# Optimization experiments

Measured on AMD Instinct MI355X. Metric: run time of the kernel, lower is better.

The kernel has to match this reference:

```python
import jax, jax.numpy as jnp
import numpy as np

ALPHA = 0.2  # LeakyReLU negative slope


def setup_inputs() -> dict:
    key = jax.random.key(0)
    k1, k2, k3, k4 = jax.random.split(key, 4)
    N, F_in, F_out = 8192, 512, 64
    x = jax.random.normal(k1, (N, F_in), dtype=jnp.float32)
    adj = jax.random.uniform(k2, (N, N), dtype=jnp.float32)
    W = jax.random.normal(k3, (F_in, F_out), dtype=jnp.float32) * 0.05
    a = jax.random.normal(k4, (2 * F_out, 1), dtype=jnp.float32) * 0.05
    return {"x": x, "adj": adj, "W": W, "a": a}


def reference(x, adj, W, a):
    F_out = W.shape[1]
    h = x @ W                                   # [N, F_out]
    # Additive attention decomposed: score[i,j] = h[i]·a1 + h[j]·a2
    # (equivalent to concat([h_i, h_j]) @ a, without the N×N×2F blowup)
    a1 = a[:F_out, 0]                           # [F_out]
    a2 = a[F_out:, 0]                           # [F_out]
    e = jax.nn.leaky_relu(h @ a1[:, None] + (h @ a2)[None, :], ALPHA)  # [N, N]
    attention = jax.nn.softmax(e * adj, axis=1)  # elementwise mult, as in source
    # dropout skipped (eval / training=False -> identity)
    h_prime = attention @ h                      # [N, F_out]
    return jax.nn.elu(h_prime)                   # concat=True branch
```

## Files before the change

kernel.cpp:

```cpp
#include <hip/hip_runtime.h>

#define ALPHA 0.2f

typedef __attribute__((ext_vector_type(8))) short short8v;
typedef __attribute__((ext_vector_type(4))) float f32x4;

__device__ __forceinline__ unsigned cvt_pk_bf16(float a, float b) {
  unsigned d;
  asm("v_cvt_pk_bf16_f32 %0, %1, %2" : "=v"(d) : "v"(a), "v"(b));
  return d;
}

__global__ __launch_bounds__(256) void k1_proj(
    const float* __restrict__ x, const float* __restrict__ W,
    const float* __restrict__ avec,
    short* __restrict__ hT, float* __restrict__ s1, float* __restrict__ s2) {
  __shared__ float xl[32 * 132];
  __shared__ float Wl[128 * 64];
  const int t   = threadIdx.x;
  const int rb  = blockIdx.x;
  const int row = t >> 3;
  const int fg  = t & 7;
  float acc[8];
#pragma unroll
  for (int e = 0; e < 8; e++) acc[e] = 0.f;

  for (int kc = 0; kc < 4; kc++) {
#pragma unroll
    for (int u = 0; u < 4; u++) {
      int lin = t + u * 256;
      int r = lin >> 5, c4 = lin & 31;
      float4 v = *(const float4*)(x + (size_t)(rb * 32 + r) * 512 + kc * 128 + c4 * 4);
      *(float4*)(xl + r * 132 + c4 * 4) = v;
    }
#pragma unroll
    for (int u = 0; u < 8; u++) {
      int lin = t + u * 256;
      int r = lin >> 4, c4 = lin & 15;
      float4 v = *(const float4*)(W + (size_t)(kc * 128 + r) * 64 + c4 * 4);
      *(float4*)(Wl + r * 64 + c4 * 4) = v;
    }
    __syncthreads();
#pragma unroll 8
    for (int k = 0; k < 128; k++) {
      float xv = xl[row * 132 + k];
      float4 w0 = *(const float4*)(Wl + k * 64 + fg * 8);
      float4 w1 = *(const float4*)(Wl + k * 64 + fg * 8 + 4);
      acc[0] = fmaf(xv, w0.x, acc[0]); acc[1] = fmaf(xv, w0.y, acc[1]);
      acc[2] = fmaf(xv, w0.z, acc[2]); acc[3] = fmaf(xv, w0.w, acc[3]);
      acc[4] = fmaf(xv, w1.x, acc[4]); acc[5] = fmaf(xv, w1.y, acc[5]);
      acc[6] = fmaf(xv, w1.z, acc[6]); acc[7] = fmaf(xv, w1.w, acc[7]);
    }
    __syncthreads();
  }

  float p1 = 0.f, p2 = 0.f;
#pragma unroll
  for (int e = 0; e < 8; e++) {
    p1 = fmaf(acc[e], avec[fg * 8 + e], p1);
    p2 = fmaf(acc[e], avec[64 + fg * 8 + e], p2);
  }
  p1 += __shfl_xor(p1, 1, 64); p1 += __shfl_xor(p1, 2, 64); p1 += __shfl_xor(p1, 4, 64);
  p2 += __shfl_xor(p2, 1, 64); p2 += __shfl_xor(p2, 2, 64); p2 += __shfl_xor(p2, 4, 64);
  const int gi = rb * 32 + row;
  if (fg == 0) { s1[gi] = p1; s2[gi] = p2; }
#pragma unroll
  for (int e = 0; e < 8; e++) {
    union { float f; unsigned u; } v; v.f = acc[e];
    unsigned rr = v.u + 0x7fffu + ((v.u >> 16) & 1u);
    hT[(size_t)(fg * 8 + e) * 8192 + gi] = (short)(rr >> 16);
  }
}

__global__ __launch_bounds__(256, 2) void k2_attn(
    const float* __restrict__ adj, const short* __restrict__ hT,
    const float* __restrict__ s1, const float* __restrict__ s2,
    float* __restrict__ num, float* __restrict__ den) {
  __shared__ short hP[32768];
  __shared__ short Pl[8192];
  const int t    = threadIdx.x;
  const int wvi  = t >> 6;
  const int l    = t & 63;
  const int lq   = l >> 4;
  const int lr   = l & 15;
  const int rb   = blockIdx.x & 127;
  const int ks   = blockIdx.x >> 7;
  const int r0   = rb << 6;
  const int j0   = ks << 9;

  float  s1own = s1[r0 + wvi * 16 + lr];
  float4 s2A4  = *(const float4*)(s2 + j0 + l * 4);
  float4 s2B4  = *(const float4*)(s2 + j0 + 256 + l * 4);

  short8v sv[16];
#pragma unroll
  for (int r = 0; r < 16; r++) {
    const int d    = r * 4096 + t * 16;
    const int frow = d >> 10;
    const int lcb  = (d & 1023) ^ ((frow & 7) << 4);
    sv[r] = *(const short8v*)(hT + (size_t)frow * 8192 + j0 + (lcb >> 1));
  }

  const float* ar = adj + (size_t)(r0 + wvi * 16) * 8192 + j0 + l * 4;
  float4 A0,A1,A2,A3,A4,A5,A6,A7,A8,A9,A10,A11,A12,A13,A14,A15;
  float4 B0,B1,B2,B3,B4,B5,B6,B7,B8,B9,B10,B11,B12,B13,B14,B15;
  A0  = *(const float4*)(ar);              B0  = *(const float4*)(ar + 256);
  A1  = *(const float4*)(ar + 1 * 8192);   B1  = *(const float4*)(ar + 1 * 8192 + 256);
  A2  = *(const float4*)(ar + 2 * 8192);   B2  = *(const float4*)(ar + 2 * 8192 + 256);
  A3  = *(const float4*)(ar + 3 * 8192);   B3  = *(const float4*)(ar + 3 * 8192 + 256);
  A4  = *(const float4*)(ar + 4 * 8192);   B4  = *(const float4*)(ar + 4 * 8192 + 256);
  A5  = *(const float4*)(ar + 5 * 8192);   B5  = *(const float4*)(ar + 5 * 8192 + 256);
  A6  = *(const float4*)(ar + 6 * 8192);   B6  = *(const float4*)(ar + 6 * 8192 + 256);
  A7  = *(const float4*)(ar + 7 * 8192);   B7  = *(const float4*)(ar + 7 * 8192 + 256);
  A8  = *(const float4*)(ar + 8 * 8192);   B8  = *(const float4*)(ar + 8 * 8192 + 256);
  A9  = *(const float4*)(ar + 9 * 8192);   B9  = *(const float4*)(ar + 9 * 8192 + 256);
  A10 = *(const float4*)(ar + 10 * 8192);  B10 = *(const float4*)(ar + 10 * 8192 + 256);
  A11 = *(const float4*)(ar + 11 * 8192);  B11 = *(const float4*)(ar + 11 * 8192 + 256);
  A12 = *(const float4*)(ar + 12 * 8192);  B12 = *(const float4*)(ar + 12 * 8192 + 256);
  A13 = *(const float4*)(ar + 13 * 8192);  B13 = *(const float4*)(ar + 13 * 8192 + 256);
  A14 = *(const float4*)(ar + 14 * 8192);  B14 = *(const float4*)(ar + 14 * 8192 + 256);
  A15 = *(const float4*)(ar + 15 * 8192);  B15 = *(const float4*)(ar + 15 * 8192 + 256);

#pragma unroll
  for (int r = 0; r < 16; r++)
    *(short8v*)((char*)hP + r * 4096 + t * 16) = sv[r];
  __syncthreads();

  float s1r[16];
#pragma unroll
  for (int i = 0; i < 16; i++) s1r[i] = __shfl(s1own, i, 64);

  float denom_p[16];
#pragma unroll
  for (int i = 0; i < 16; i++) denom_p[i] = 0.f;
  f32x4 acc[4];
#pragma unroll
  for (int fb = 0; fb < 4; fb++) acc[fb] = (f32x4){0.f, 0.f, 0.f, 0.f};

  char* Pw = (char*)Pl + wvi * 4096;
  unsigned pk0[16], pk1[16];

#define EXPROW4(I, AV, S2V) do {                                              \
    float z0 = s1r[I] + S2V.x; z0 = fmaxf(z0, ALPHA * z0) * AV.x;             \
    float z1 = s1r[I] + S2V.y; z1 = fmaxf(z1, ALPHA * z1) * AV.y;             \
    float z2 = s1r[I] + S2V.z; z2 = fmaxf(z2, ALPHA * z2) * AV.z;             \
    float z3 = s1r[I] + S2V.w; z3 = fmaxf(z3, ALPHA * z3) * AV.w;             \
    float w0 = __expf(z0), w1 = __expf(z1), w2 = __expf(z2), w3 = __expf(z3); \
    denom_p[I] += (w0 + w1) + (w2 + w3);                                      \
    pk0[I] = cvt_pk_bf16(w0, w1); pk1[I] = cvt_pk_bf16(w2, w3);               \
  } while (0)

#define PWRITE(HALF) do {                                                     \
    if ((l >> 5) == (HALF)) {                                                 \
      const int cb = (l & 31) * 8;                                            \
      _Pragma("unroll")                                                       \
      for (int i2 = 0; i2 < 16; i2++) {                                       \
        uint2 pv; pv.x = pk0[i2]; pv.y = pk1[i2];                             \
        *(uint2*)(Pw + (((i2 << 8) + cb) ^ ((i2 & 7) << 4))) = pv;            \
      }                                                                       \
    }                                                                         \
  } while (0)

#define MFMACHUNK(CL) do {                                                    \
    __builtin_amdgcn_s_setprio(1);                                            \
    _Pragma("unroll")                                                         \
    for (int kk = 0; kk < 4; kk++) {                                          \
      const int ab = ((lr << 8) + (kk << 6) + (lq << 4)) ^ ((lr & 7) << 4);   \
      const short8v au = *(const short8v*)(Pw + ab);                          \
      _Pragma("unroll")                                                       \
      for (int fb = 0; fb < 4; fb++) {                                        \
        const int fr = fb * 16 + lr;                                          \
        const int bb = ((fr << 10) + ((CL) << 8) + (kk << 6) + (lq << 4))     \
                       ^ ((fr & 7) << 4);                                     \
        const short8v bu = *(const short8v*)((char*)hP + bb);                 \
        acc[fb] = __builtin_amdgcn_mfma_f32_16x16x32_bf16(au, bu,             \
                                                          acc[fb], 0, 0, 0); \
      }                                                                       \
    }                                                                         \
    __builtin_amdgcn_s_setprio(0);                                            \
  } while (0)

  EXPROW4(0, A0, s2A4);   EXPROW4(1, A1, s2A4);   EXPROW4(2, A2, s2A4);
  EXPROW4(3, A3, s2A4);   EXPROW4(4, A4, s2A4);   EXPROW4(5, A5, s2A4);
  EXPROW4(6, A6, s2A4);   EXPROW4(7, A7, s2A4);   EXPROW4(8, A8, s2A4);
  EXPROW4(9, A9, s2A4);   EXPROW4(10, A10, s2A4); EXPROW4(11, A11, s2A4);
  EXPROW4(12, A12, s2A4); EXPROW4(13, A13, s2A4); EXPROW4(14, A14, s2A4);
  EXPROW4(15, A15, s2A4);
  PWRITE(0); MFMACHUNK(0);
  PWRITE(1); MFMACHUNK(1);

  EXPROW4(0, B0, s2B4);   EXPROW4(1, B1, s2B4);   EXPROW4(2, B2, s2B4);
  EXPROW4(3, B3, s2B4);   EXPROW4(4, B4, s2B4);   EXPROW4(5, B5, s2B4);
  EXPROW4(6, B6, s2B4);   EXPROW4(7, B7, s2B4);   EXPROW4(8, B8, s2B4);
  EXPROW4(9, B9, s2B4);   EXPROW4(10, B10, s2B4); EXPROW4(11, B11, s2B4);
  EXPROW4(12, B12, s2B4); EXPROW4(13, B13, s2B4); EXPROW4(14, B14, s2B4);
  EXPROW4(15, B15, s2B4);
  PWRITE(0); MFMACHUNK(2);
  PWRITE(1); MFMACHUNK(3);

#undef EXPROW4
#undef PWRITE
#undef MFMACHUNK

#pragma unroll
  for (int i = 0; i < 16; i++) {
    float d = denom_p[i];
    d += __shfl_xor(d, 1, 64); d += __shfl_xor(d, 2, 64);
    d += __shfl_xor(d, 4, 64); d += __shfl_xor(d, 8, 64);
    d += __shfl_xor(d, 16, 64); d += __shfl_xor(d, 32, 64);
    if (l == 0) den[(size_t)ks * 8192 + r0 + wvi * 16 + i] = d;
  }
  float* np = num + (size_t)ks * 524288;
#pragma unroll
  for (int fb = 0; fb < 4; fb++)
#pragma unroll
    for (int r = 0; r < 4; r++)
      np[(size_t)(r0 + wvi * 16 + lq * 4 + r) * 64 + fb * 16 + lr] = acc[fb][r];
}

__global__ __launch_bounds__(256) void k3_norm(
    const float* __restrict__ num, const float* __restrict__ den,
    float* __restrict__ out) {
  const int idx = blockIdx.x * 256 + threadIdx.x;
  const int row = idx >> 6;
  float n = 0.f, d = 0.f;
#pragma unroll
  for (int ksi = 0; ksi < 16; ksi++) {
    n += num[(size_t)ksi * 524288 + idx];
    d += den[ksi * 8192 + row];
  }
  float v = n / d;
  out[idx] = v > 0.f ? v : (__expf(v) - 1.f);
}

extern "C" void kernel_launch(void* const* d_in, const int* in_sizes, int n_in,
                              void* d_out, int out_size, void* d_ws, size_t ws_size,
                              hipStream_t stream) {
  const float* x   = (const float*)d_in[0];
  const float* adj = (const float*)d_in[1];
  const float* W   = (const float*)d_in[2];
  const float* av  = (const float*)d_in[3];
  float* out = (float*)d_out;
  char* ws = (char*)d_ws;

  short* hT  = (short*)ws;
  float* s1  = (float*)(ws + (1 << 20));
  float* s2  = (float*)(ws + (1 << 20) + 32768);
  float* num = (float*)(ws + (1 << 20) + 65536);
  float* den = num + 16u * 524288u;

  hipLaunchKernelGGL(k1_proj, dim3(256), dim3(256), 0, stream, x, W, av, hT, s1, s2);
  hipLaunchKernelGGL(k2_attn, dim3(2048), dim3(256), 0, stream,
                     adj, hT, s1, s2, num, den);
  hipLaunchKernelGGL(k3_norm, dim3(2048), dim3(256), 0, stream, num, den, out);
}
```

Measured before the change: 101.1 us.

## Load hT directly to LDS, split adj loads, and atomically reduce numerators

The k2 staging of hT now uses global_load_lds to copy straight into shared memory, skipping the register round trip. The adj loads are split so the B half is issued after the barrier, which lowers peak register pressure. Partial numerators from the 16 K-splits are combined with float atomicAdd into one zero-initialized buffer (zeroed in k1), so k3 reads one numerator instead of 16. The atomics add contention and make the summation order nondeterministic.

```diff
diff --git a/kernel.cpp b/kernel.cpp
--- a/kernel.cpp
+++ b/kernel.cpp
@@ -11,16 +11,29 @@
   return d;
 }
 
+#define GLOAD_LDS16(gp, lp)                                                   \
+  __builtin_amdgcn_global_load_lds(                                           \
+      (const __attribute__((address_space(1))) unsigned int*)(gp),            \
+      (__attribute__((address_space(3))) unsigned int*)(lp), 16, 0, 0)
+
 __global__ __launch_bounds__(256) void k1_proj(
     const float* __restrict__ x, const float* __restrict__ W,
     const float* __restrict__ avec,
-    short* __restrict__ hT, float* __restrict__ s1, float* __restrict__ s2) {
+    short* __restrict__ hT, float* __restrict__ s1, float* __restrict__ s2,
+    float* __restrict__ num) {
   __shared__ float xl[32 * 132];
   __shared__ float Wl[128 * 64];
   const int t   = threadIdx.x;
   const int rb  = blockIdx.x;
   const int row = t >> 3;
   const int fg  = t & 7;
+
+  {
+    float4 z = {0.f, 0.f, 0.f, 0.f};
+    *(float4*)(num + rb * 2048 + t * 8)     = z;
+    *(float4*)(num + rb * 2048 + t * 8 + 4) = z;
+  }
+
   float acc[8];
 #pragma unroll
   for (int e = 0; e < 8; e++) acc[e] = 0.f;
@@ -92,39 +105,53 @@
   float4 s2A4  = *(const float4*)(s2 + j0 + l * 4);
   float4 s2B4  = *(const float4*)(s2 + j0 + 256 + l * 4);
 
-  short8v sv[16];
 #pragma unroll
   for (int r = 0; r < 16; r++) {
     const int d    = r * 4096 + t * 16;
     const int frow = d >> 10;
     const int lcb  = (d & 1023) ^ ((frow & 7) << 4);
-    sv[r] = *(const short8v*)(hT + (size_t)frow * 8192 + j0 + (lcb >> 1));
+    GLOAD_LDS16(hT + (size_t)frow * 8192 + j0 + (lcb >> 1), (char*)hP + d);
   }
 
   const float* ar = adj + (size_t)(r0 + wvi * 16) * 8192 + j0 + l * 4;
   float4 A0,A1,A2,A3,A4,A5,A6,A7,A8,A9,A10,A11,A12,A13,A14,A15;
+  A0  = *(const float4*)(ar);
+  A1  = *(const float4*)(ar + 1 * 8192);
+  A2  = *(const float4*)(ar + 2 * 8192);
+  A3  = *(const float4*)(ar + 3 * 8192);
+  A4  = *(const float4*)(ar + 4 * 8192);
+  A5  = *(const float4*)(ar + 5 * 8192);
+  A6  = *(const float4*)(ar + 6 * 8192);
+  A7  = *(const float4*)(ar + 7 * 8192);
+  A8  = *(const float4*)(ar + 8 * 8192);
+  A9  = *(const float4*)(ar + 9 * 8192);
+  A10 = *(const float4*)(ar + 10 * 8192);
+  A11 = *(const float4*)(ar + 11 * 8192);
+  A12 = *(const float4*)(ar + 12 * 8192);
+  A13 = *(const float4*)(ar + 13 * 8192);
+  A14 = *(const float4*)(ar + 14 * 8192);
+  A15 = *(const float4*)(ar + 15 * 8192);
+
+  __syncthreads();
+  __builtin_amdgcn_sched_barrier(0);
+
   float4 B0,B1,B2,B3,B4,B5,B6,B7,B8,B9,B10,B11,B12,B13,B14,B15;
-  A0  = *(const float4*)(ar);              B0  = *(const float4*)(ar + 256);
-  A1  = *(const float4*)(ar + 1 * 8192);   B1  = *(const float4*)(ar + 1 * 8192 + 256);
-  A2  = *(const float4*)(ar + 2 * 8192);   B2  = *(const float4*)(ar + 2 * 8192 + 256);
-  A3  = *(const float4*)(ar + 3 * 8192);   B3  = *(const float4*)(ar + 3 * 8192 + 256);
-  A4  = *(const float4*)(ar + 4 * 8192);   B4  = *(const float4*)(ar + 4 * 8192 + 256);
-  A5  = *(const float4*)(ar + 5 * 8192);   B5  = *(const float4*)(ar + 5 * 8192 + 256);
-  A6  = *(const float4*)(ar + 6 * 8192);   B6  = *(const float4*)(ar + 6 * 8192 + 256);
-  A7  = *(const float4*)(ar + 7 * 8192);   B7  = *(const float4*)(ar + 7 * 8192 + 256);
-  A8  = *(const float4*)(ar + 8 * 8192);   B8  = *(const float4*)(ar + 8 * 8192 + 256);
-  A9  = *(const float4*)(ar + 9 * 8192);   B9  = *(const float4*)(ar + 9 * 8192 + 256);
-  A10 = *(const float4*)(ar + 10 * 8192);  B10 = *(const float4*)(ar + 10 * 8192 + 256);
-  A11 = *(const float4*)(ar + 11 * 8192);  B11 = *(const float4*)(ar + 11 * 8192 + 256);
-  A12 = *(const float4*)(ar + 12 * 8192);  B12 = *(const float4*)(ar + 12 * 8192 + 256);
-  A13 = *(const float4*)(ar + 13 * 8192);  B13 = *(const float4*)(ar + 13 * 8192 + 256);
-  A14 = *(const float4*)(ar + 14 * 8192);  B14 = *(const float4*)(ar + 14 * 8192 + 256);
-  A15 = *(const float4*)(ar + 15 * 8192);  B15 = *(const float4*)(ar + 15 * 8192 + 256);
-
-#pragma unroll
-  for (int r = 0; r < 16; r++)
-    *(short8v*)((char*)hP + r * 4096 + t * 16) = sv[r];
-  __syncthreads();
+  B0  = *(const float4*)(ar + 256);
+  B1  = *(const float4*)(ar + 1 * 8192 + 256);
+  B2  = *(const float4*)(ar + 2 * 8192 + 256);
+  B3  = *(const float4*)(ar + 3 * 8192 + 256);
+  B4  = *(const float4*)(ar + 4 * 8192 + 256);
+  B5  = *(const float4*)(ar + 5 * 8192 + 256);
+  B6  = *(const float4*)(ar + 6 * 8192 + 256);
+  B7  = *(const float4*)(ar + 7 * 8192 + 256);
+  B8  = *(const float4*)(ar + 8 * 8192 + 256);
+  B9  = *(const float4*)(ar + 9 * 8192 + 256);
+  B10 = *(const float4*)(ar + 10 * 8192 + 256);
+  B11 = *(const float4*)(ar + 11 * 8192 + 256);
+  B12 = *(const float4*)(ar + 12 * 8192 + 256);
+  B13 = *(const float4*)(ar + 13 * 8192 + 256);
+  B14 = *(const float4*)(ar + 14 * 8192 + 256);
+  B15 = *(const float4*)(ar + 15 * 8192 + 256);
 
   float s1r[16];
 #pragma unroll
@@ -210,12 +237,12 @@
     d += __shfl_xor(d, 16, 64); d += __shfl_xor(d, 32, 64);
     if (l == 0) den[(size_t)ks * 8192 + r0 + wvi * 16 + i] = d;
   }
-  float* np = num + (size_t)ks * 524288;
 #pragma unroll
   for (int fb = 0; fb < 4; fb++)
 #pragma unroll
     for (int r = 0; r < 4; r++)
-      np[(size_t)(r0 + wvi * 16 + lq * 4 + r) * 64 + fb * 16 + lr] = acc[fb][r];
+      atomicAdd(&num[(size_t)(r0 + wvi * 16 + lq * 4 + r) * 64 + fb * 16 + lr],
+                acc[fb][r]);
 }
 
 __global__ __launch_bounds__(256) void k3_norm(
@@ -223,13 +250,10 @@
     float* __restrict__ out) {
   const int idx = blockIdx.x * 256 + threadIdx.x;
   const int row = idx >> 6;
-  float n = 0.f, d = 0.f;
-#pragma unroll
-  for (int ksi = 0; ksi < 16; ksi++) {
-    n += num[(size_t)ksi * 524288 + idx];
-    d += den[ksi * 8192 + row];
-  }
-  float v = n / d;
+  float d = 0.f;
+#pragma unroll
+  for (int ksi = 0; ksi < 16; ksi++) d += den[ksi * 8192 + row];
+  float v = num[idx] / d;
   out[idx] = v > 0.f ? v : (__expf(v) - 1.f);
 }
 
@@ -247,9 +271,10 @@
   float* s1  = (float*)(ws + (1 << 20));
   float* s2  = (float*)(ws + (1 << 20) + 32768);
   float* num = (float*)(ws + (1 << 20) + 65536);
-  float* den = num + 16u * 524288u;
-
-  hipLaunchKernelGGL(k1_proj, dim3(256), dim3(256), 0, stream, x, W, av, hT, s1, s2);
+  float* den = num + 524288u;
+
+  hipLaunchKernelGGL(k1_proj, dim3(256), dim3(256), 0, stream,
+                     x, W, av, hT, s1, s2, num);
   hipLaunchKernelGGL(k2_attn, dim3(2048), dim3(256), 0, stream,
                      adj, hT, s1, s2, num, den);
   hipLaunchKernelGGL(k3_norm, dim3(2048), dim3(256), 0, stream, num, den, out);
```

New measurement: 90.85 us. 1.11x faster.
